# Performance work log

Measured on AMD Instinct MI355X. Metric: run time of the kernel, lower is better.

## Reference

```python
import jax, jax.numpy as jnp
import numpy as np

B, LMAX, T_OUT, VOCAB, EMB, CVEC, HID, OUT = 8192, 12, 10, 36, 300, 256, 256, 512


def setup_inputs() -> dict:
    key = jax.random.key(0)
    ks = jax.random.split(key, 16)
    s = lambda fan: 1.0 / np.sqrt(fan)
    u = lambda k, shape, b: jax.random.uniform(k, shape, jnp.float32, -b, b)
    inp = {
        'words': jax.random.randint(ks[0], (B, LMAX), 0, VOCAB),
        'lengths': 1 + jax.random.randint(ks[1], (B,), 0, LMAX),  # in [1, LMAX]
        'emb_table': jax.random.normal(ks[2], (VOCAB, EMB), jnp.float32),
        'enc_w': u(ks[3], (CVEC, EMB), s(EMB)),
        'enc_b': u(ks[4], (CVEC,), s(EMB)),
        'wih_f': u(ks[5], (4 * HID, CVEC), s(HID)),
        'whh_f': u(ks[6], (4 * HID, HID), s(HID)),
        'bih_f': u(ks[7], (4 * HID,), s(HID)),
        'bhh_f': u(ks[8], (4 * HID,), s(HID)),
        'wih_b': u(ks[9], (4 * HID, CVEC), s(HID)),
        'whh_b': u(ks[10], (4 * HID, HID), s(HID)),
        'bih_b': u(ks[11], (4 * HID,), s(HID)),
        'bhh_b': u(ks[12], (4 * HID,), s(HID)),
        'out_w': u(ks[13], (OUT, 2 * HID), s(2 * HID)),
        'out_b': u(ks[14], (OUT,), s(2 * HID)),
    }
    return inp


def _interp_words(emb_table, words, lengths):
    # bilinear resize (L,300)->(10,300) with align_corners=True; width unchanged
    # so it is exact linear interpolation along the char axis.
    def one(word_row, L):
        Lf = (L - 1).astype(jnp.float32)
        pos = jnp.arange(T_OUT, dtype=jnp.float32) * Lf / (T_OUT - 1)  # (10,)
        i0 = jnp.floor(pos).astype(jnp.int32)
        i1 = jnp.minimum(i0 + 1, L - 1).astype(jnp.int32)
        f = (pos - i0.astype(jnp.float32))[:, None]
        e = emb_table[word_row]  # (LMAX, EMB)
        return e[i0] * (1.0 - f) + e[i1] * f  # (10, EMB)
    return jax.vmap(one)(words, lengths)  # (B, 10, EMB)


def _lstm(seq, wih, whh, bih, bhh):
    # seq: (T, B, In); PyTorch gate order i, f, g, o
    bsz = seq.shape[1]
    h0 = jnp.zeros((bsz, HID), seq.dtype)
    c0 = jnp.zeros((bsz, HID), seq.dtype)

    def step(carry, x_t):
        h, c = carry
        g = x_t @ wih.T + h @ whh.T + (bih + bhh)
        i, f, gg, o = jnp.split(g, 4, axis=-1)
        c = jax.nn.sigmoid(f) * c + jax.nn.sigmoid(i) * jnp.tanh(gg)
        h = jax.nn.sigmoid(o) * jnp.tanh(c)
        return (h, c), h

    _, hs = jax.lax.scan(step, (h0, c0), seq)
    return hs  # (T, B, HID)


def reference(words, lengths, emb_table, enc_w, enc_b, wih_f, whh_f, bih_f, bhh_f,
              wih_b, whh_b, bih_b, bhh_b, out_w, out_b):
    emb = _interp_words(emb_table, words, lengths)              # (B, 10, 300)
    cv = jax.nn.relu(emb @ enc_w.T + enc_b)                     # (B, 10, 256)
    seq = jnp.transpose(cv, (1, 0, 2))                          # (10, B, 256)
    h_f = _lstm(seq, wih_f, whh_f, bih_f, bhh_f)                # (10, B, 256)
    h_b = _lstm(seq[::-1], wih_b, whh_b, bih_b, bhh_b)[::-1]    # (10, B, 256)
    rec = jnp.concatenate([h_f, h_b], axis=-1)                  # (10, B, 512)
    out = rec @ out_w.T + out_b                                 # (10, B, 512)
    return jnp.transpose(out, (1, 0, 2))                        # (B, 10, 512)
```

## Files before the change

kernel.cpp:

```cpp
#include <hip/hip_runtime.h>
#include <hip/hip_fp16.h>

typedef _Float16 f16;
typedef _Float16 f16x2 __attribute__((ext_vector_type(2)));
typedef _Float16 f16x8 __attribute__((ext_vector_type(8)));
typedef float    f32x4 __attribute__((ext_vector_type(4)));

#define NB   8192
#define TOUT 10
#define LMAX 12
#define EMB  300

__device__ __forceinline__ float sigm_(float x) {
    return __builtin_amdgcn_rcpf(1.0f + __builtin_amdgcn_exp2f(x * -1.44269504f));
}
__device__ __forceinline__ float tanh_(float x) {
    return 1.0f - 2.0f * __builtin_amdgcn_rcpf(1.0f + __builtin_amdgcn_exp2f(x * 2.88539008f));
}
__device__ __forceinline__ f16x2 pk_f16(float a, float b) {
    return __builtin_bit_cast(f16x2, __builtin_amdgcn_cvt_pkrtz(a, b));
}

__device__ __forceinline__ void gl_lds16(const f16* g, f16* l) {
    __builtin_amdgcn_global_load_lds(
        (const __attribute__((address_space(1))) void*)g,
        (__attribute__((address_space(3))) void*)l, 16, 0, 0);
}

__global__ __launch_bounds__(256) void pack_w2(
    const float* __restrict__ wih_f, const float* __restrict__ whh_f,
    const float* __restrict__ wih_b, const float* __restrict__ whh_b,
    f16* __restrict__ Wp) {
    int idx = blockIdx.x * 256 + threadIdx.x;
    int d   = idx >> 19;
    int r   = idx & 524287;
    int tile = r >> 9;
    int e    = r & 511;
    int kc = tile >> 6, nt = tile & 63;
    int khi = e >> 7, rem = e & 127, nl = rem >> 3, klo = rem & 7;
    int n = nt * 16 + nl;
    int k = kc * 32 + khi * 8 + klo;
    int w = n >> 7, rr = n & 127, gate = rr >> 5;
    int u = w * 32 + 2 * (rr & 15) + ((rr >> 4) & 1);
    int srow = gate * 256 + u;
    const float* wih = d ? wih_b : wih_f;
    const float* whh = d ? whh_b : whh_f;
    float v = (k < 256) ? wih[srow * 256 + k] : whh[srow * 256 + (k - 256)];
    Wp[idx] = (f16)v;
}

__global__ __launch_bounds__(256) void pack_bias(
    const float* __restrict__ bih_f, const float* __restrict__ bhh_f,
    const float* __restrict__ bih_b, const float* __restrict__ bhh_b,
    float* __restrict__ bp) {
    int idx = blockIdx.x * 256 + threadIdx.x;
    int d = idx >> 10, n = idx & 1023;
    int w = n >> 7, rr = n & 127, gate = rr >> 5;
    int u = w * 32 + 2 * (rr & 15) + ((rr >> 4) & 1);
    int srow = gate * 256 + u;
    bp[idx] = d ? (bih_b[srow] + bhh_b[srow]) : (bih_f[srow] + bhh_f[srow]);
}

__global__ __launch_bounds__(256) void pack_w3(
    const float* __restrict__ out_w, f16* __restrict__ W3p) {
    int idx = blockIdx.x * 256 + threadIdx.x;
    int tile = idx >> 9, e = idx & 511;
    int kc = tile >> 5, nt = tile & 31;
    int khi = e >> 7, rem = e & 127, nl = rem >> 3, klo = rem & 7;
    int n = nt * 16 + nl, k = kc * 32 + khi * 8 + klo;
    W3p[idx] = (f16)out_w[n * 512 + k];
}

__global__ __launch_bounds__(256) void enc_proj(
    const float* __restrict__ tab, const float* __restrict__ ew,
    const float* __restrict__ eb, float* __restrict__ P) {
    int v = blockIdx.x, j = threadIdx.x;
    const float* a = tab + v * EMB;
    const float* w = ew + j * EMB;
    float s = 0.0f;
    for (int k = 0; k < EMB; ++k) s += a[k] * w[k];
    P[v * 256 + j] = s + eb[j];
}

__global__ __launch_bounds__(256) void build_seq(
    const int* __restrict__ words, const int* __restrict__ lengths,
    const float* __restrict__ P, f16* __restrict__ seqp) {
    int gi = blockIdx.x * 256 + threadIdx.x;
    int bl  = gi & 15;
    int khi = (gi >> 4) & 3;
    int kc  = (gi >> 6) & 7;
    int mt  = (gi >> 9) & 511;
    int t   = gi >> 18;
    int b = mt * 16 + bl;
    int L = lengths[b];
    float pos = ((float)t * (float)(L - 1)) / 9.0f;
    int i0 = (int)pos;
    float f = pos - (float)i0;
    int i1 = min(i0 + 1, L - 1);
    int c0 = words[b * LMAX + i0];
    int c1 = words[b * LMAX + i1];
    const float* p0 = P + c0 * 256 + kc * 32 + khi * 8;
    const float* p1 = P + c1 * 256 + kc * 32 + khi * 8;
    f16x8 r;
#pragma unroll
    for (int j = 0; j < 8; ++j) {
        float v = p0[j] * (1.0f - f) + p1[j] * f;
        v = fmaxf(v, 0.0f);
        r[j] = (f16)v;
    }
    *((f16x8*)seqp + gi) = r;
}

__global__ __launch_bounds__(512) void lstm_fused(
    const f16* __restrict__ seqp, const f16* __restrict__ Wp,
    const float* __restrict__ bp, f16* __restrict__ hcat) {
    const int dir  = blockIdx.x >> 7;
    const int r0t  = (blockIdx.x & 127) << 2;
    const int wave = threadIdx.x >> 6;
    const int lane = threadIdx.x & 63;
    const int l16  = lane & 15;
    const int quad = lane >> 4;

    __shared__ __align__(16) f16 hbuf[2][16384];
    __shared__ __align__(16) f16 sbuf[2][16384];

    {
        f16x8 z = {(f16)0, (f16)0, (f16)0, (f16)0, (f16)0, (f16)0, (f16)0, (f16)0};
        for (int i = threadIdx.x; i < 2048; i += 512) ((f16x8*)hbuf[0])[i] = z;
    }

    {
        const int t0 = dir ? 9 : 0;
        const f16* s0 = seqp + (size_t)(t0 * 512 + r0t) * 4096;
#pragma unroll
        for (int r = 0; r < 4; ++r)
            gl_lds16(s0 + r * 4096 + threadIdx.x * 8, &sbuf[0][r * 4096 + wave * 512]);
    }

    const float* bpd = bp + dir * 1024 + wave * 128;
    float bias_l[8];
#pragma unroll
    for (int nt = 0; nt < 8; ++nt) bias_l[nt] = bpd[nt * 16 + l16];

    const f16* Wdl = Wp + dir * 524288 + wave * 4096 + lane * 8;

    const int wt0 = ((l16 >> 2) * 16 + quad * 4) * 8 + 2 * (l16 & 3);
    const int tile_lo = (r0t * 16 + dir * 8 + wave) * 512;

    float cst[4][4][2];
#pragma unroll
    for (int m = 0; m < 4; ++m)
#pragma unroll
        for (int q = 0; q < 4; ++q) { cst[m][q][0] = 0.0f; cst[m][q][1] = 0.0f; }

    __syncthreads();

    int cur = 0;
#pragma unroll 1
    for (int step = 0; step < TOUT; ++step) {
        const int t = dir ? (9 - step) : step;
        const f16* hb_r = hbuf[cur] + lane * 8;
        const f16* sb   = sbuf[cur] + lane * 8;
        f16*       hb_w = hbuf[cur ^ 1];

        f16x8 bA[4], bB[4];
#pragma unroll
        for (int nt = 0; nt < 4; ++nt)
            bA[nt] = *(const f16x8*)(Wdl + 8 * 32768 + nt * 512);
#pragma unroll
        for (int nt = 0; nt < 4; ++nt)
            bB[nt] = *(const f16x8*)(Wdl + 8 * 32768 + (nt + 4) * 512);

        if (step != 9) {
            const int tn = dir ? (t - 1) : (t + 1);
            const f16* ns = seqp + (size_t)(tn * 512 + r0t) * 4096;
#pragma unroll
            for (int r = 0; r < 4; ++r)
                gl_lds16(ns + r * 4096 + threadIdx.x * 8,
                         &sbuf[cur ^ 1][r * 4096 + wave * 512]);
        }

        f32x4 acc[4][8];
#pragma unroll
        for (int m = 0; m < 4; ++m)
#pragma unroll
            for (int nt = 0; nt < 8; ++nt)
#pragma unroll
                for (int q = 0; q < 4; ++q) acc[m][nt][q] = bias_l[nt];

#pragma unroll 1
        for (int j = 0; j < 16; ++j) {
            const int c = j & 7;
            const f16* ab = (j < 8) ? hb_r : sb;
            f16x8 aA[4];
#pragma unroll
            for (int m = 0; m < 4; ++m)
                aA[m] = *(const f16x8*)(ab + (m * 8 + c) * 512);

            __builtin_amdgcn_s_setprio(1);
#pragma unroll
            for (int m = 0; m < 4; ++m)
#pragma unroll
                for (int nt = 0; nt < 4; ++nt)
                    acc[m][nt] = __builtin_amdgcn_mfma_f32_16x16x32_f16(
                        aA[m], bA[nt], acc[m][nt], 0, 0, 0);
            __builtin_amdgcn_s_setprio(0);

            if (j < 15) {
                const int kcn = (j + 1) ^ 8;
#pragma unroll
                for (int nt = 0; nt < 4; ++nt)
                    bA[nt] = *(const f16x8*)(Wdl + kcn * 32768 + nt * 512);
            }

            __builtin_amdgcn_s_setprio(1);
#pragma unroll
            for (int m = 0; m < 4; ++m)
#pragma unroll
                for (int nt = 0; nt < 4; ++nt)
                    acc[m][nt + 4] = __builtin_amdgcn_mfma_f32_16x16x32_f16(
                        aA[m], bB[nt], acc[m][nt + 4], 0, 0, 0);
            __builtin_amdgcn_s_setprio(0);

            if (j < 15) {
                const int kcn = (j + 1) ^ 8;
#pragma unroll
                for (int nt = 0; nt < 4; ++nt)
                    bB[nt] = *(const f16x8*)(Wdl + kcn * 32768 + (nt + 4) * 512);
            }
        }

        f16* hct = hcat + ((size_t)t * 4194304 + tile_lo);
#pragma unroll
        for (int m = 0; m < 4; ++m) {
#pragma unroll
            for (int q = 0; q < 4; ++q) {
                float i0 = acc[m][0][q], i1 = acc[m][1][q];
                float f0 = acc[m][2][q], f1 = acc[m][3][q];
                float g0 = acc[m][4][q], g1 = acc[m][5][q];
                float o0 = acc[m][6][q], o1 = acc[m][7][q];
                float c0 = sigm_(f0) * cst[m][q][0] + sigm_(i0) * tanh_(g0);
                float c1 = sigm_(f1) * cst[m][q][1] + sigm_(i1) * tanh_(g1);
                cst[m][q][0] = c0;
                cst[m][q][1] = c1;
                float h0 = sigm_(o0) * tanh_(c0);
                float h1 = sigm_(o1) * tanh_(c1);
                f16x2 hv = pk_f16(h0, h1);
                int wt = wt0 + q * 8;
                *(f16x2*)&hb_w[(m * 8 + wave) * 512 + wt] = hv;
                *(f16x2*)(hct + m * 8192 + wt) = hv;
            }
        }

        __syncthreads();
        cur ^= 1;
    }
}

__global__ __launch_bounds__(512) void out_gemm(
    const f16* __restrict__ hcat, const f16* __restrict__ W3p,
    const float* __restrict__ out_b, float* __restrict__ out) {
    const int mt0  = blockIdx.x << 2;
    const int wave = threadIdx.x >> 6;
    const int lane = threadIdx.x & 63;
    const int l16  = lane & 15;
    const int quad = lane >> 4;
    const int n0   = wave * 64;

    float bias_l[4];
#pragma unroll
    for (int nt = 0; nt < 4; ++nt) bias_l[nt] = out_b[n0 + nt * 16 + l16];

    f32x4 acc[4][4];
#pragma unroll
    for (int m = 0; m < 4; ++m)
#pragma unroll
        for (int nt = 0; nt < 4; ++nt)
#pragma unroll
            for (int q = 0; q < 4; ++q) acc[m][nt][q] = bias_l[nt];

#pragma unroll 2
    for (int kc = 0; kc < 16; ++kc) {
        f16x8 a[4], b[4];
#pragma unroll
        for (int m = 0; m < 4; ++m)
            a[m] = *(const f16x8*)(hcat + ((size_t)((mt0 + m) * 16 + kc) * 512 + lane * 8));
#pragma unroll
        for (int nt = 0; nt < 4; ++nt)
            b[nt] = *(const f16x8*)(W3p + ((kc * 32 + wave * 4 + nt) * 512 + lane * 8));
#pragma unroll
        for (int m = 0; m < 4; ++m)
#pragma unroll
            for (int nt = 0; nt < 4; ++nt)
                acc[m][nt] = __builtin_amdgcn_mfma_f32_16x16x32_f16(a[m], b[nt], acc[m][nt], 0, 0, 0);
    }

#pragma unroll
    for (int m = 0; m < 4; ++m) {
#pragma unroll
        for (int nt = 0; nt < 4; ++nt) {
#pragma unroll
            for (int q = 0; q < 4; ++q) {
                int R = mt0 * 16 + m * 16 + quad * 4 + q;
                int t = R >> 13;
                int b = R & 8191;
                out[(size_t)(b * 10 + t) * 512 + n0 + nt * 16 + l16] = acc[m][nt][q];
            }
        }
    }
}

extern "C" void kernel_launch(void* const* d_in, const int* in_sizes, int n_in,
                              void* d_out, int out_size, void* d_ws, size_t ws_size,
                              hipStream_t stream) {
    const int*   words   = (const int*)d_in[0];
    const int*   lengths = (const int*)d_in[1];
    const float* tab     = (const float*)d_in[2];
    const float* enc_w   = (const float*)d_in[3];
    const float* enc_b   = (const float*)d_in[4];
    const float* wih_f   = (const float*)d_in[5];
    const float* whh_f   = (const float*)d_in[6];
    const float* bih_f   = (const float*)d_in[7];
    const float* bhh_f   = (const float*)d_in[8];
    const float* wih_b   = (const float*)d_in[9];
    const float* whh_b   = (const float*)d_in[10];
    const float* bih_b   = (const float*)d_in[11];
    const float* bhh_b   = (const float*)d_in[12];
    const float* out_w   = (const float*)d_in[13];
    const float* out_b   = (const float*)d_in[14];
    float* out = (float*)d_out;

    char* ws = (char*)d_ws;
    f16*   Wp   = (f16*)(ws + 0);
    f16*   W3p  = (f16*)(ws + 2097152);
    float* bp   = (float*)(ws + 2621440);
    float* P    = (float*)(ws + 2629632);
    f16*   seqp = (f16*)(ws + 2666496);
    f16*   hcat = (f16*)(ws + 44609536);

    pack_w2<<<4096, 256, 0, stream>>>(wih_f, whh_f, wih_b, whh_b, Wp);
    pack_bias<<<8, 256, 0, stream>>>(bih_f, bhh_f, bih_b, bhh_b, bp);
    pack_w3<<<1024, 256, 0, stream>>>(out_w, W3p);
    enc_proj<<<36, 256, 0, stream>>>(tab, enc_w, enc_b, P);
    build_seq<<<10240, 256, 0, stream>>>(words, lengths, P, seqp);
    lstm_fused<<<256, 512, 0, stream>>>(seqp, Wp, bp, hcat);
    out_gemm<<<1280, 512, 0, stream>>>(hcat, W3p, out_b, out);
}
```

Before: 477.3 us.

## Fully unroll LSTM K-loop with triple-buffered weight prefetch across steps

Replaces the runtime 16-iteration K loop in the fused LSTM kernel with a fully unrolled sequence of 32 half-steps. It rotates three register buffers for weight fragments so each load is issued two MFMA groups ahead of use, and it preloads the first weight tiles for the next timestep before the gate epilogue and the barrier. The goal is to hide global weight-load latency behind MFMA work. In exchange it raises VGPR pressure and code size, which could cause spills or lower occupancy.

Result: slower. 961.3 us (+101.4%).

```diff
diff --git a/kernel.cpp b/kernel.cpp
--- a/kernel.cpp
+++ b/kernel.cpp
@@ -26,6 +26,8 @@
         (const __attribute__((address_space(1))) void*)g,
         (__attribute__((address_space(3))) void*)l, 16, 0, 0);
 }
+
+#define MF(a, b, c) __builtin_amdgcn_mfma_f32_16x16x32_f16(a, b, c, 0, 0, 0)
 
 __global__ __launch_bounds__(256) void pack_w2(
     const float* __restrict__ wih_f, const float* __restrict__ whh_f,
@@ -128,7 +130,6 @@
         f16x8 z = {(f16)0, (f16)0, (f16)0, (f16)0, (f16)0, (f16)0, (f16)0, (f16)0};
         for (int i = threadIdx.x; i < 2048; i += 512) ((f16x8*)hbuf[0])[i] = z;
     }
-
     {
         const int t0 = dir ? 9 : 0;
         const f16* s0 = seqp + (size_t)(t0 * 512 + r0t) * 4096;
@@ -153,7 +154,39 @@
 #pragma unroll
         for (int q = 0; q < 4; ++q) { cst[m][q][0] = 0.0f; cst[m][q][1] = 0.0f; }
 
+    f16x8 S0[4], S1[4], S2[4];
+#pragma unroll
+    for (int nt = 0; nt < 4; ++nt) S0[nt] = *(const f16x8*)(Wdl + 8 * 32768 + nt * 512);
+#pragma unroll
+    for (int nt = 0; nt < 4; ++nt) S1[nt] = *(const f16x8*)(Wdl + 8 * 32768 + (4 + nt) * 512);
+
     __syncthreads();
+
+#define HSTEP(P, SC, SD) do {                                                  \
+    if ((P) < 30) {                                                            \
+        const f16* ws_ = Wdl + (((((P) + 2) >> 1) ^ 8) * 32768                 \
+                                + (((P) + 2) & 1) * 2048);                     \
+        _Pragma("unroll")                                                      \
+        for (int nt_ = 0; nt_ < 4; ++nt_)                                      \
+            SD[nt_] = *(const f16x8*)(ws_ + nt_ * 512);                        \
+    }                                                                          \
+    if (((P) & 1) == 0) {                                                      \
+        const f16* ab_ = ((P) < 16) ? hb_r : sb;                               \
+        const int c_ = ((P) >> 1) & 7;                                         \
+        _Pragma("unroll")                                                      \
+        for (int m_ = 0; m_ < 4; ++m_)                                         \
+            aA[m_] = *(const f16x8*)(ab_ + (m_ * 8 + c_) * 512);               \
+    }                                                                          \
+    __builtin_amdgcn_s_setprio(1);                                             \
+    _Pragma("unroll")                                                          \
+    for (int m_ = 0; m_ < 4; ++m_) {                                           \
+        _Pragma("unroll")                                                      \
+        for (int nt_ = 0; nt_ < 4; ++nt_)                                      \
+            acc[m_][((P) & 1) * 4 + nt_] =                                     \
+                MF(aA[m_], SC[nt_], acc[m_][((P) & 1) * 4 + nt_]);             \
+    }                                                                          \
+    __builtin_amdgcn_s_setprio(0);                                             \
+} while (0)
 
     int cur = 0;
 #pragma unroll 1
@@ -163,13 +196,32 @@
         const f16* sb   = sbuf[cur] + lane * 8;
         f16*       hb_w = hbuf[cur ^ 1];
 
-        f16x8 bA[4], bB[4];
-#pragma unroll
-        for (int nt = 0; nt < 4; ++nt)
-            bA[nt] = *(const f16x8*)(Wdl + 8 * 32768 + nt * 512);
-#pragma unroll
-        for (int nt = 0; nt < 4; ++nt)
-            bB[nt] = *(const f16x8*)(Wdl + 8 * 32768 + (nt + 4) * 512);
+        f32x4 acc[4][8];
+#pragma unroll
+        for (int m = 0; m < 4; ++m)
+#pragma unroll
+            for (int nt = 0; nt < 8; ++nt)
+#pragma unroll
+                for (int q = 0; q < 4; ++q) acc[m][nt][q] = bias_l[nt];
+
+        f16x8 aA[4];
+
+        HSTEP(0, S0, S2);  HSTEP(1, S1, S0);  HSTEP(2, S2, S1);
+        HSTEP(3, S0, S2);  HSTEP(4, S1, S0);  HSTEP(5, S2, S1);
+        HSTEP(6, S0, S2);  HSTEP(7, S1, S0);  HSTEP(8, S2, S1);
+        HSTEP(9, S0, S2);  HSTEP(10, S1, S0); HSTEP(11, S2, S1);
+        HSTEP(12, S0, S2); HSTEP(13, S1, S0); HSTEP(14, S2, S1);
+        HSTEP(15, S0, S2); HSTEP(16, S1, S0); HSTEP(17, S2, S1);
+        HSTEP(18, S0, S2); HSTEP(19, S1, S0); HSTEP(20, S2, S1);
+        HSTEP(21, S0, S2); HSTEP(22, S1, S0); HSTEP(23, S2, S1);
+        HSTEP(24, S0, S2); HSTEP(25, S1, S0); HSTEP(26, S2, S1);
+        HSTEP(27, S0, S2); HSTEP(28, S1, S0); HSTEP(29, S2, S1);
+        HSTEP(30, S0, S2); HSTEP(31, S1, S0);
+
+#pragma unroll
+        for (int nt = 0; nt < 4; ++nt) S0[nt] = *(const f16x8*)(Wdl + 8 * 32768 + nt * 512);
+#pragma unroll
+        for (int nt = 0; nt < 4; ++nt) S1[nt] = *(const f16x8*)(Wdl + 8 * 32768 + (4 + nt) * 512);
 
         if (step != 9) {
             const int tn = dir ? (t - 1) : (t + 1);
@@ -178,56 +230,6 @@
             for (int r = 0; r < 4; ++r)
                 gl_lds16(ns + r * 4096 + threadIdx.x * 8,
                          &sbuf[cur ^ 1][r * 4096 + wave * 512]);
-        }
-
-        f32x4 acc[4][8];
-#pragma unroll
-        for (int m = 0; m < 4; ++m)
-#pragma unroll
-            for (int nt = 0; nt < 8; ++nt)
-#pragma unroll
-                for (int q = 0; q < 4; ++q) acc[m][nt][q] = bias_l[nt];
-
-#pragma unroll 1
-        for (int j = 0; j < 16; ++j) {
-            const int c = j & 7;
-            const f16* ab = (j < 8) ? hb_r : sb;
-            f16x8 aA[4];
-#pragma unroll
-            for (int m = 0; m < 4; ++m)
-                aA[m] = *(const f16x8*)(ab + (m * 8 + c) * 512);
-
-            __builtin_amdgcn_s_setprio(1);
-#pragma unroll
-            for (int m = 0; m < 4; ++m)
-#pragma unroll
-                for (int nt = 0; nt < 4; ++nt)
-                    acc[m][nt] = __builtin_amdgcn_mfma_f32_16x16x32_f16(
-                        aA[m], bA[nt], acc[m][nt], 0, 0, 0);
-            __builtin_amdgcn_s_setprio(0);
-
-            if (j < 15) {
-                const int kcn = (j + 1) ^ 8;
-#pragma unroll
-                for (int nt = 0; nt < 4; ++nt)
-                    bA[nt] = *(const f16x8*)(Wdl + kcn * 32768 + nt * 512);
-            }
-
-            __builtin_amdgcn_s_setprio(1);
-#pragma unroll
-            for (int m = 0; m < 4; ++m)
-#pragma unroll
-                for (int nt = 0; nt < 4; ++nt)
-                    acc[m][nt + 4] = __builtin_amdgcn_mfma_f32_16x16x32_f16(
-                        aA[m], bB[nt], acc[m][nt + 4], 0, 0, 0);
-            __builtin_amdgcn_s_setprio(0);
-
-            if (j < 15) {
-                const int kcn = (j + 1) ^ 8;
-#pragma unroll
-                for (int nt = 0; nt < 4; ++nt)
-                    bB[nt] = *(const f16x8*)(Wdl + kcn * 32768 + (nt + 4) * 512);
-            }
         }
 
         f16* hct = hcat + ((size_t)t * 4194304 + tile_lo);
@@ -255,6 +257,7 @@
         __syncthreads();
         cur ^= 1;
     }
+#undef HSTEP
 }
 
 __global__ __launch_bounds__(512) void out_gemm(
@@ -292,7 +295,7 @@
         for (int m = 0; m < 4; ++m)
 #pragma unroll
             for (int nt = 0; nt < 4; ++nt)
-                acc[m][nt] = __builtin_amdgcn_mfma_f32_16x16x32_f16(a[m], b[nt], acc[m][nt], 0, 0, 0);
+                acc[m][nt] = MF(a[m], b[nt], acc[m][nt]);
     }
 
 #pragma unroll
```
